# Kernel optimization log

Hardware: AMD Instinct MI355X
Metric: run time of the kernel (lower is better)

## Reference

```python
import jax, jax.numpy as jnp
import numpy as np

N = 50_000        # nodes
E = 1_600_000     # edges (avg degree 32)
H = 64            # hidden_channels
DEPTH = 3         # -> 2*DEPTH mid conv layers


def setup_inputs() -> dict:
    key = jax.random.key(0)
    ks = jax.random.split(key, 8)
    x = jax.random.normal(ks[0], (N, 1), dtype=jnp.float32)
    edge_index = jax.random.randint(ks[1], (2, E), 0, N, dtype=jnp.int32)
    s = 0.1  # small init scale
    W_in = s * jax.random.normal(ks[2], (2 * 1 + 1, H), dtype=jnp.float32)
    b_in = jnp.zeros((H,), jnp.float32)
    W_mid = s * jax.random.normal(ks[3], (2 * DEPTH, 2 * H + 1, H), dtype=jnp.float32)
    b_mid = jnp.zeros((2 * DEPTH, H), jnp.float32)
    W_out = s * jax.random.normal(ks[4], (2 * H + 1, 1), dtype=jnp.float32)
    b_out = jnp.zeros((1,), jnp.float32)
    return {"x": x, "edge_index": edge_index, "W_in": W_in, "b_in": b_in,
            "W_mid": W_mid, "b_mid": b_mid, "W_out": W_out, "b_out": b_out}


def _conv(x, src, dst, sign, inv_deg, W, b):
    """Directional_EdgeConv: mean_{j->i} Linear([x_i, x_j - x_i, sign(j-i)])."""
    x_i = x[dst]                                   # [E, F] target feats
    x_j = x[src]                                   # [E, F] source feats
    feat = jnp.concatenate([x_i, x_j - x_i, sign], axis=-1)  # [E, 2F+1]
    msg = feat @ W + b                             # [E, out]
    agg = jax.ops.segment_sum(msg, dst, num_segments=x.shape[0])  # [N, out]
    return agg * inv_deg                           # mean aggregation


def reference(x, edge_index, W_in, b_in, W_mid, b_mid, W_out, b_out):
    src = edge_index[0]
    dst = edge_index[1]
    # vectorized replacement of the per-edge Python sign loop
    sign = jnp.sign((src - dst).astype(x.dtype))[:, None]        # [E, 1]
    deg = jax.ops.segment_sum(jnp.ones((src.shape[0],), x.dtype), dst,
                              num_segments=x.shape[0])
    inv_deg = (1.0 / jnp.maximum(deg, 1.0))[:, None]             # [N, 1]

    x2 = _conv(x, src, dst, sign, inv_deg, W_in, b_in)
    for l in range(DEPTH):
        x1 = jax.nn.leaky_relu(
            _conv(x2, src, dst, sign, inv_deg, W_mid[2 * l], b_mid[2 * l]))
        x2 = jax.nn.leaky_relu(
            _conv(x1, src, dst, sign, inv_deg, W_mid[2 * l + 1], b_mid[2 * l + 1]) + x2)
    return _conv(x2, src, dst, sign, inv_deg, W_out, b_out) + x
```

## Files before the change

### kernel.cpp

```cpp
#include <hip/hip_runtime.h>
#include <hip/hip_fp16.h>

#define HDIM 64
#define NEG_SLOPE 0.01f
#define CAPB 8192
#define BCAP 6144
#define EPB  4096

typedef _Float16 half8 __attribute__((ext_vector_type(8)));
typedef float f32x4 __attribute__((ext_vector_type(4)));

static __device__ __forceinline__ float h_lo(unsigned d) {
    return __half2float(__ushort_as_half((unsigned short)(d & 0xffffu)));
}
static __device__ __forceinline__ float h_hi(unsigned d) {
    return __half2float(__ushort_as_half((unsigned short)(d >> 16)));
}
static __device__ __forceinline__ unsigned packh(float a, float b) {
    unsigned short ra = __half_as_ushort(__float2half(a));
    unsigned short rb = __half_as_ushort(__float2half(b));
    return ((unsigned)rb << 16) | (unsigned)ra;
}
static __device__ __forceinline__ half8 u4h(uint4 v) {
    union { uint4 u; half8 h; } x; x.u = v; return x.h;
}
static __device__ __forceinline__ __half2 uh2(unsigned u) {
    union { unsigned u; __half2 h; } x; x.u = u; return x.h;
}

__global__ void k_setup(int ptotal, const float* __restrict__ W_mid,
                        unsigned short* __restrict__ WTh,
                        int NB, int* gcur, int N, unsigned* xAP, unsigned* xBP,
                        float* tvec) {
    int i = blockIdx.x * blockDim.x + threadIdx.x;
    if (i < ptotal) {
        int l = i >> 13;
        int rem = i & 8191;
        int h = rem >> 7;
        int k = rem & 127;
        const float* W = W_mid + (size_t)l * 129 * 64;
        float v = W[k * 64 + h] - ((k < 64) ? W[(64 + k) * 64 + h] : 0.f);
        WTh[i] = __half_as_ushort(__float2half(v));
    }
    if (i < NB) gcur[i] = i * CAPB;
    if (i < 32) xAP[(size_t)N * 32 + i] = 0u;
    else if (i < 64) xBP[(size_t)N * 32 + (i - 32)] = 0u;
    else if (i == 64) tvec[N] = 0.f;
}

__global__ __launch_bounds__(1024) void k_bucket(
        int E, const int* __restrict__ src, const int* __restrict__ dst,
        int* gcur, unsigned* __restrict__ bucketed, int NB) {
    __shared__ int lh[512];
    __shared__ int sd[512];
    __shared__ int lbase[512];
    __shared__ unsigned sorted[EPB];
    int t = threadIdx.x;
    int e0 = blockIdx.x * EPB;
    if (t < 512) lh[t] = 0;
    __syncthreads();
    int dv[4], sv[4], rv[4];
#pragma unroll
    for (int k = 0; k < 4; ++k) {
        int e = e0 + k * 1024 + t;
        dv[k] = (e < E) ? dst[e] : -1;
        sv[k] = (e < E) ? src[e] : 0;
    }
#pragma unroll
    for (int k = 0; k < 4; ++k)
        rv[k] = (dv[k] >= 0) ? atomicAdd(&lh[((unsigned)dv[k]) >> 7], 1) : 0;
    __syncthreads();
    int c = (t < 512) ? lh[t] : 0;
    if (t < 512) {
        lbase[t] = (c > 0) ? atomicAdd(&gcur[t], c) : 0;
        sd[t] = c;
    }
    __syncthreads();
    int x = c;
    for (int s = 1; s < 512; s <<= 1) {
        int p = (t < 512 && t >= s) ? sd[t - s] : 0;
        __syncthreads();
        if (t < 512) { x += p; sd[t] = x; }
        __syncthreads();
    }
#pragma unroll
    for (int k = 0; k < 4; ++k) {
        if (dv[k] >= 0) {
            int b = ((unsigned)dv[k]) >> 7;
            sorted[sd[b] - lh[b] + rv[k]] = ((unsigned)dv[k] << 16) | (unsigned)sv[k];
        }
    }
    __syncthreads();
    int ntot = sd[511];
    for (int i = t; i < ntot; i += 1024) {
        unsigned w = sorted[i];
        int b = (int)(w >> 23);
        int pos = lbase[b] + (i - (sd[b] - lh[b]));
        if (pos < (b + 1) * CAPB) bucketed[pos] = w;
    }
}

__global__ __launch_bounds__(512) void k_csr(
        int N, int NB, const unsigned* __restrict__ bucketed, const int* __restrict__ gcur,
        unsigned short* __restrict__ csr, unsigned short* __restrict__ pcsr,
        int* __restrict__ rowptr, float* __restrict__ ssinv) {
    __shared__ unsigned st[BCAP];
    __shared__ int hist[128], cur[128], excl[128], sgp[128];
    __shared__ int gsd[512];
    int b = blockIdx.x, t = threadIdx.x;
    int n0 = b << 7;
    int nn = min(128, N - n0);
    int cc = (t < NB) ? min(gcur[t] - t * CAPB, CAPB) : 0;
    gsd[t] = cc;
    __syncthreads();
    int xs = cc;
    for (int s = 1; s < 512; s <<= 1) {
        int p = (t >= s) ? gsd[t - s] : 0;
        __syncthreads();
        xs += p;
        gsd[t] = xs;
        __syncthreads();
    }
    int cnt = min(gcur[b] - b * CAPB, CAPB);
    int base = gsd[b] - cnt;
    if (b == NB - 1 && t == 0) rowptr[N] = gsd[NB - 1];
    if (t < 128) { hist[t] = 0; sgp[t] = 0; }
    unsigned sent = ((unsigned)N << 16) | (unsigned)N;
    unsigned* pb32 = (unsigned*)(pcsr + ((size_t)b << 13));
    for (int i = t; i < 4096; i += 512) pb32[i] = sent;
    __syncthreads();
    bool single = (cnt <= BCAP);
    for (int off = 0; off < cnt; off += BCAP) {
        int bs = min(BCAP, cnt - off);
        for (int i = t; i < bs; i += 512) {
            unsigned w = bucketed[b * CAPB + off + i];
            if (single) st[i] = w;
            int d = (int)(w >> 16);
            int s = (int)(w & 0xffffu);
            int dl = d - n0;
            atomicAdd(&hist[dl], 1);
            atomicAdd(&sgp[dl], ((s < d) ? 1024 : 0) + ((s == d) ? 1 : 0));
        }
    }
    __syncthreads();
    int deg_t = (t < 128) ? hist[t] : 0;
    int x = deg_t;
    for (int s = 1; s < 128; s <<= 1) {
        int p = (t < 128 && t >= s) ? hist[t - s] : 0;
        __syncthreads();
        if (t < 128) { x += p; hist[t] = x; }
        __syncthreads();
    }
    if (t < 128) {
        int ex = hist[t] - deg_t;
        excl[t] = ex;
        cur[t] = ex;
        if (t < nn) {
            rowptr[n0 + t] = base + ex;
            int sg = sgp[t];
            int lt = sg >> 10, eq = sg & 1023;
            float ss = (float)(deg_t - eq - 2 * lt);
            ssinv[n0 + t] = (deg_t > 0) ? ss / (float)deg_t : 0.f;
        }
    }
    __syncthreads();
    for (int off = 0; off < cnt; off += BCAP) {
        int bs = min(BCAP, cnt - off);
        if (!single) {
            for (int i = t; i < bs; i += 512) st[i] = bucketed[b * CAPB + off + i];
            __syncthreads();
        }
        for (int i = t; i < bs; i += 512) {
            unsigned w = st[i];
            int dl = (int)(w >> 16) - n0;
            unsigned short sval = (unsigned short)(w & 0xffffu);
            int p = atomicAdd(&cur[dl], 1);
            csr[base + p] = sval;
            int r = p - excl[dl];
            if (r < 64) pcsr[((size_t)(n0 + dl) << 6) + r] = sval;
        }
        if (!single) __syncthreads();
    }
}

__global__ void k_in(int N, const float* __restrict__ x0,
                     const int* __restrict__ rowptr, const unsigned short* __restrict__ csr,
                     const float* __restrict__ ssinv,
                     const float* __restrict__ W_in, const float* __restrict__ b_in,
                     unsigned* __restrict__ xoutP) {
    int wid = blockIdx.x * (blockDim.x >> 6) + (threadIdx.x >> 6);
    int lane = threadIdx.x & 63;
    if (wid >= N) return;
    int beg = rowptr[wid], end = rowptr[wid + 1];
    int deg = end - beg;
    float s = 0.f;
    for (int e = beg + lane; e < end; e += 64) s += x0[csr[e]];
    for (int m = 32; m >= 1; m >>= 1) s += __shfl_xor(s, m, 64);
    float invd = 1.f / (float)max(deg, 1);
    float mean = s * invd;
    float xi = x0[wid];
    float w1 = W_in[lane], w2 = W_in[64 + lane], w3 = W_in[128 + lane];
    float y = xi * (w1 - w2) + mean * w2 + ssinv[wid] * w3 + b_in[lane];
    if (deg == 0) y = 0.f;
    float ylo = __shfl(y, (2 * lane) & 63, 64);
    float yhi = __shfl(y, (2 * lane + 1) & 63, 64);
    unsigned pkd = packh(ylo, yhi);
    if (lane < 32) xoutP[(size_t)wid * 32 + lane] = pkd;
}

static __device__ __forceinline__ void chunk_acc(
        const uint4* __restrict__ xin16, int sv, int base, int sub, int lq,
        __half2& c0, __half2& c1, __half2& c2, __half2& c3) {
    int s0 = __shfl(sv, base + sub, 64);
    int s1 = __shfl(sv, base + 8 + sub, 64);
    int s2 = __shfl(sv, base + 16 + sub, 64);
    int s3 = __shfl(sv, base + 24 + sub, 64);
    uint4 d0 = xin16[(size_t)s0 * 8 + lq];
    uint4 d1 = xin16[(size_t)s1 * 8 + lq];
    uint4 d2 = xin16[(size_t)s2 * 8 + lq];
    uint4 d3 = xin16[(size_t)s3 * 8 + lq];
    c0 = __hadd2(c0, __hadd2(__hadd2(uh2(d0.x), uh2(d1.x)), __hadd2(uh2(d2.x), uh2(d3.x))));
    c1 = __hadd2(c1, __hadd2(__hadd2(uh2(d0.y), uh2(d1.y)), __hadd2(uh2(d2.y), uh2(d3.y))));
    c2 = __hadd2(c2, __hadd2(__hadd2(uh2(d0.z), uh2(d1.z)), __hadd2(uh2(d2.z), uh2(d3.z))));
    c3 = __hadd2(c3, __hadd2(__hadd2(uh2(d0.w), uh2(d1.w)), __hadd2(uh2(d2.w), uh2(d3.w))));
}

static __device__ __forceinline__ void slow_gather(
        const uint4* __restrict__ xin16, const unsigned short* __restrict__ csr,
        int beg, int end, int N, int lane, int sub, int lq, float* a) {
#pragma unroll
    for (int j = 0; j < 8; ++j) a[j] = 0.f;
    for (int tb = beg; tb < end; tb += 64) {
        int cnt = min(64, end - tb);
        int sv = (lane < cnt) ? (int)csr[tb + lane] : N;
        int ng = (cnt + 7) >> 3;
        for (int g = 0; g < ng; ++g) {
            int si = __shfl(sv, (g << 3) + sub, 64);
            uint4 d = xin16[(size_t)si * 8 + lq];
            a[0] += h_lo(d.x); a[1] += h_hi(d.x);
            a[2] += h_lo(d.y); a[3] += h_hi(d.y);
            a[4] += h_lo(d.z); a[5] += h_hi(d.z);
            a[6] += h_lo(d.w); a[7] += h_hi(d.w);
        }
    }
#pragma unroll
    for (int m = 8; m <= 32; m <<= 1) {
#pragma unroll
        for (int j = 0; j < 8; ++j) a[j] += __shfl_xor(a[j], m, 64);
    }
}

template <bool RES, bool TOUT>
__global__ __launch_bounds__(256) void k_layer(
        int N, const unsigned* __restrict__ xinP,
        const unsigned* __restrict__ xresP, unsigned* __restrict__ xoutP,
        const int* __restrict__ rowptr, const unsigned short* __restrict__ csr,
        const unsigned short* __restrict__ pcsr,
        const float* __restrict__ ssinv,
        const unsigned short* __restrict__ WThl,
        const float* __restrict__ W3, const float* __restrict__ bias,
        const float* __restrict__ Wt, float* __restrict__ tvec) {
    __shared__ unsigned Ald[16 * 64];
    __shared__ float Cld[16 * 64];
    __shared__ int sdeg[16];
    __shared__ float sss[16];

    int t = threadIdx.x;
    int lane = t & 63;
    int wv = t >> 6;
    int n0 = blockIdx.x << 4;
    int kg = lane >> 4;

    int cb = (wv << 4) + (lane & 15);
    const uint4* wp = (const uint4*)WThl;
    uint4 b0 = wp[cb * 16 + kg + 0];
    uint4 b1 = wp[cb * 16 + kg + 4];
    uint4 b2 = wp[cb * 16 + kg + 8];
    uint4 b3 = wp[cb * 16 + kg + 12];

    const uint4* xin16 = (const uint4*)xinP;
    int sub = lane >> 3;
    int lq = lane & 7;
    int ndb = wv << 2;

    int svp[4];
#pragma unroll
    for (int q = 0; q < 4; ++q)
        svp[q] = (int)pcsr[((size_t)(n0 + ndb + q) << 6) + lane];

#pragma unroll
    for (int qp = 0; qp < 2; ++qp) {
        int ndA = ndb + (qp << 1);
        int ndB = ndA + 1;
        int nodeA = n0 + ndA, nodeB = n0 + ndB;
        int ncA = min(nodeA, N - 1), ncB = min(nodeB, N - 1);
        int begA = __builtin_amdgcn_readfirstlane(rowptr[ncA]);
        int endA = __builtin_amdgcn_readfirstlane(rowptr[ncA + 1]);
        int begB = __builtin_amdgcn_readfirstlane(rowptr[ncB]);
        int endB = __builtin_amdgcn_readfirstlane(rowptr[ncB + 1]);
        int degA = (nodeA < N) ? (endA - begA) : 0;
        int degB = (nodeB < N) ? (endB - begB) : 0;
        float ssvA = ssinv[ncA];
        float ssvB = ssinv[ncB];
        uint4 xiA = make_uint4(0u, 0u, 0u, 0u), xiB = make_uint4(0u, 0u, 0u, 0u);
        if (lane < 8) {
            if (nodeA < N) xiA = xin16[(size_t)ncA * 8 + lane];
            if (nodeB < N) xiB = xin16[(size_t)ncB * 8 + lane];
        }
        uint4 mvA, mvB;
        if (max(degA, degB) <= 64) {
            __half2 z = uh2(0u);
            __half2 cA0 = z, cA1 = z, cA2 = z, cA3 = z;
            __half2 cB0 = z, cB1 = z, cB2 = z, cB3 = z;
            int svA = svp[qp << 1], svB = svp[(qp << 1) + 1];
            chunk_acc(xin16, svA, 0, sub, lq, cA0, cA1, cA2, cA3);
            chunk_acc(xin16, svB, 0, sub, lq, cB0, cB1, cB2, cB3);
            if (degA > 32) chunk_acc(xin16, svA, 32, sub, lq, cA0, cA1, cA2, cA3);
            if (degB > 32) chunk_acc(xin16, svB, 32, sub, lq, cB0, cB1, cB2, cB3);
#pragma unroll
            for (int m = 8; m <= 32; m <<= 1) {
                cA0 = __hadd2(cA0, uh2((unsigned)__shfl_xor((int)*(unsigned*)&cA0, m, 64)));
                cA1 = __hadd2(cA1, uh2((unsigned)__shfl_xor((int)*(unsigned*)&cA1, m, 64)));
                cA2 = __hadd2(cA2, uh2((unsigned)__shfl_xor((int)*(unsigned*)&cA2, m, 64)));
                cA3 = __hadd2(cA3, uh2((unsigned)__shfl_xor((int)*(unsigned*)&cA3, m, 64)));
                cB0 = __hadd2(cB0, uh2((unsigned)__shfl_xor((int)*(unsigned*)&cB0, m, 64)));
                cB1 = __hadd2(cB1, uh2((unsigned)__shfl_xor((int)*(unsigned*)&cB1, m, 64)));
                cB2 = __hadd2(cB2, uh2((unsigned)__shfl_xor((int)*(unsigned*)&cB2, m, 64)));
                cB3 = __hadd2(cB3, uh2((unsigned)__shfl_xor((int)*(unsigned*)&cB3, m, 64)));
            }
            float idA = 1.f / (float)max(degA, 1);
            float idB = 1.f / (float)max(degB, 1);
            mvA.x = packh(__half2float(__low2half(cA0)) * idA, __half2float(__high2half(cA0)) * idA);
            mvA.y = packh(__half2float(__low2half(cA1)) * idA, __half2float(__high2half(cA1)) * idA);
            mvA.z = packh(__half2float(__low2half(cA2)) * idA, __half2float(__high2half(cA2)) * idA);
            mvA.w = packh(__half2float(__low2half(cA3)) * idA, __half2float(__high2half(cA3)) * idA);
            mvB.x = packh(__half2float(__low2half(cB0)) * idB, __half2float(__high2half(cB0)) * idB);
            mvB.y = packh(__half2float(__low2half(cB1)) * idB, __half2float(__high2half(cB1)) * idB);
            mvB.z = packh(__half2float(__low2half(cB2)) * idB, __half2float(__high2half(cB2)) * idB);
            mvB.w = packh(__half2float(__low2half(cB3)) * idB, __half2float(__high2half(cB3)) * idB);
        } else {
            float aA[8], aB[8];
            slow_gather(xin16, csr, begA, endA, N, lane, sub, lq, aA);
            slow_gather(xin16, csr, begB, endB, N, lane, sub, lq, aB);
            float idA = 1.f / (float)max(degA, 1);
            float idB = 1.f / (float)max(degB, 1);
            mvA.x = packh(aA[0] * idA, aA[1] * idA);
            mvA.y = packh(aA[2] * idA, aA[3] * idA);
            mvA.z = packh(aA[4] * idA, aA[5] * idA);
            mvA.w = packh(aA[6] * idA, aA[7] * idA);
            mvB.x = packh(aB[0] * idB, aB[1] * idB);
            mvB.y = packh(aB[2] * idB, aB[3] * idB);
            mvB.z = packh(aB[4] * idB, aB[5] * idB);
            mvB.w = packh(aB[6] * idB, aB[7] * idB);
        }
        if (lane < 8) {
            int gxA = lane ^ (ndA & 7), gmA = (8 + lane) ^ (ndA & 7);
            int gxB = lane ^ (ndB & 7), gmB = (8 + lane) ^ (ndB & 7);
            ((uint4*)Ald)[ndA * 16 + gxA] = xiA;
            ((uint4*)Ald)[ndA * 16 + gmA] = mvA;
            ((uint4*)Ald)[ndB * 16 + gxB] = xiB;
            ((uint4*)Ald)[ndB * 16 + gmB] = mvB;
        }
        if (lane == 0) {
            sdeg[ndA] = degA; sss[ndA] = ssvA;
            sdeg[ndB] = degB; sss[ndB] = ssvB;
        }
    }
    __syncthreads();

    int r = lane & 15;
    const uint4* ap = (const uint4*)Ald;
    int rx = (r & 7);
    uint4 fa0 = ap[r * 16 + ((0 + kg) ^ rx)];
    uint4 fa1 = ap[r * 16 + ((4 + kg) ^ rx)];
    uint4 fa2 = ap[r * 16 + ((8 + kg) ^ rx)];
    uint4 fa3 = ap[r * 16 + ((12 + kg) ^ rx)];
    f32x4 acc = {0.f, 0.f, 0.f, 0.f};
    acc = __builtin_amdgcn_mfma_f32_16x16x32_f16(u4h(fa0), u4h(b0), acc, 0, 0, 0);
    acc = __builtin_amdgcn_mfma_f32_16x16x32_f16(u4h(fa1), u4h(b1), acc, 0, 0, 0);
    acc = __builtin_amdgcn_mfma_f32_16x16x32_f16(u4h(fa2), u4h(b2), acc, 0, 0, 0);
    acc = __builtin_amdgcn_mfma_f32_16x16x32_f16(u4h(fa3), u4h(b3), acc, 0, 0, 0);
#pragma unroll
    for (int reg = 0; reg < 4; ++reg)
        Cld[(kg * 4 + reg) * 64 + (wv << 4) + r] = acc[reg];
    __syncthreads();

    int nd = t >> 4;
    int node = n0 + nd;
    if (node < N) {
        int dg = sdeg[nd];
        float ss = sss[nd];
        float tp = 0.f;
#pragma unroll
        for (int jj = 0; jj < 2; ++jj) {
            int j = (t & 15) + jj * 16;
            float y0 = Cld[nd * 64 + 2 * j];
            float y1 = Cld[nd * 64 + 2 * j + 1];
            float2 w3 = ((const float2*)W3)[j];
            float2 bb = ((const float2*)bias)[j];
            y0 += ss * w3.x + bb.x;
            y1 += ss * w3.y + bb.y;
            if (dg == 0) { y0 = 0.f; y1 = 0.f; }
            if (RES) {
                unsigned rw = xresP[(size_t)node * 32 + j];
                y0 += h_lo(rw);
                y1 += h_hi(rw);
            }
            y0 = (y0 > 0.f) ? y0 : NEG_SLOPE * y0;
            y1 = (y1 > 0.f) ? y1 : NEG_SLOPE * y1;
            if (TOUT) {
                float2 wt = ((const float2*)Wt)[j];
                tp += y0 * wt.x + y1 * wt.y;
            }
            xoutP[(size_t)node * 32 + j] = packh(y0, y1);
        }
        if (TOUT) {
            tp += __shfl_xor(tp, 1, 64);
            tp += __shfl_xor(tp, 2, 64);
            tp += __shfl_xor(tp, 4, 64);
            tp += __shfl_xor(tp, 8, 64);
            if ((t & 15) == 0) tvec[node] = tp;
        }
    }
}

__global__ void k_out(int N, const unsigned* __restrict__ xAP, const float* __restrict__ x0,
                      const int* __restrict__ rowptr, const unsigned short* __restrict__ csr,
                      const unsigned short* __restrict__ pcsr,
                      const float* __restrict__ ssinv, const float* __restrict__ t,
                      const float* __restrict__ W_out, const float* __restrict__ b_out,
                      float* __restrict__ out) {
    int wid = blockIdx.x * (blockDim.x >> 6) + (threadIdx.x >> 6);
    int lane = threadIdx.x & 63;
    if (wid >= N) return;
    int beg = rowptr[wid], end = rowptr[wid + 1];
    int deg = end - beg;
    float s;
    if (deg <= 64) {
        int sl = (int)pcsr[((size_t)wid << 6) + lane];
        s = t[sl];
    } else {
        s = 0.f;
        for (int e = beg + lane; e < end; e += 64) s += t[csr[e]];
    }
    unsigned xw = xAP[(size_t)wid * 32 + (lane >> 1)];
    float xf = (lane & 1) ? h_hi(xw) : h_lo(xw);
    float p = xf * (W_out[lane] - W_out[64 + lane]);
    for (int m = 32; m >= 1; m >>= 1) {
        s += __shfl_xor(s, m, 64);
        p += __shfl_xor(p, m, 64);
    }
    float invd = 1.f / (float)max(deg, 1);
    float y = p + s * invd + ssinv[wid] * W_out[128] + b_out[0];
    if (deg == 0) y = 0.f;
    if (lane == 0) out[wid] = y + x0[wid];
}

static inline size_t align16(size_t x) { return (x + 15) & ~(size_t)15; }

extern "C" void kernel_launch(void* const* d_in, const int* in_sizes, int n_in,
                              void* d_out, int out_size, void* d_ws, size_t ws_size,
                              hipStream_t stream) {
    const float* x0    = (const float*)d_in[0];
    const int*   ei    = (const int*)d_in[1];
    const float* W_in  = (const float*)d_in[2];
    const float* b_in  = (const float*)d_in[3];
    const float* W_mid = (const float*)d_in[4];
    const float* b_mid = (const float*)d_in[5];
    const float* W_out = (const float*)d_in[6];
    const float* b_out = (const float*)d_in[7];
    float* out = (float*)d_out;

    const int N = in_sizes[0];
    const int E = in_sizes[1] / 2;
    const int L = in_sizes[4] / (129 * 64);
    const int NB = (N + 127) >> 7;
    const int* src = ei;
    const int* dst = ei + E;

    char* p = (char*)d_ws;
    unsigned short* WTh = (unsigned short*)p; p += align16((size_t)L * 64 * 128 * 2);
    unsigned* xAP = (unsigned*)p; p += align16((size_t)(N + 1) * 32 * 4);
    unsigned* xBP = (unsigned*)p; p += align16((size_t)(N + 1) * 32 * 4);
    unsigned* bucketed = (unsigned*)p; p += align16((size_t)NB * CAPB * 4);
    unsigned short* csr = (unsigned short*)p; p += align16((size_t)E * 2);
    unsigned short* pcsr = (unsigned short*)p; p += align16((size_t)NB * 8192 * 2);
    int* gcur          = (int*)p; p += align16((size_t)(NB + 1) * 4);
    int* rowptr        = (int*)p; p += align16((size_t)(N + 1) * 4);
    float* ssinv       = (float*)p; p += align16((size_t)N * 4);
    float* t           = (float*)p; p += align16((size_t)(N + 1) * 4);

    const int nb_w4 = (N + 3) / 4;
    const int nb_bkt = (E + EPB - 1) / EPB;
    const int ptotal = L * 64 * 128;
    const int nb_lay = (N + 15) / 16;

    k_setup<<<(ptotal + 255) / 256, 256, 0, stream>>>(ptotal, W_mid, WTh, NB, gcur, N, xAP, xBP, t);
    k_bucket<<<nb_bkt, 1024, 0, stream>>>(E, src, dst, gcur, bucketed, NB);
    k_csr<<<NB, 512, 0, stream>>>(N, NB, bucketed, gcur, csr, pcsr, rowptr, ssinv);

    k_in<<<nb_w4, 256, 0, stream>>>(N, x0, rowptr, csr, ssinv, W_in, b_in, xAP);

    for (int l = 0; l < L / 2; ++l) {
        bool last = (l == L / 2 - 1);
        const unsigned short* Wa = WTh + (size_t)(2 * l) * 64 * 128;
        const unsigned short* Wb = WTh + (size_t)(2 * l + 1) * 64 * 128;
        const float* W3a = W_mid + (size_t)(2 * l) * 129 * 64 + 128 * 64;
        const float* W3b = W_mid + (size_t)(2 * l + 1) * 129 * 64 + 128 * 64;

        k_layer<false, false><<<nb_lay, 256, 0, stream>>>(
            N, xAP, nullptr, xBP, rowptr, csr, pcsr, ssinv,
            Wa, W3a, b_mid + (size_t)(2 * l) * HDIM, nullptr, nullptr);
        if (!last) {
            k_layer<true, false><<<nb_lay, 256, 0, stream>>>(
                N, xBP, xAP, xAP, rowptr, csr, pcsr, ssinv,
                Wb, W3b, b_mid + (size_t)(2 * l + 1) * HDIM, nullptr, nullptr);
        } else {
            k_layer<true, true><<<nb_lay, 256, 0, stream>>>(
                N, xBP, xAP, xAP, rowptr, csr, pcsr, ssinv,
                Wb, W3b, b_mid + (size_t)(2 * l + 1) * HDIM, W_out + 64, t);
        }
    }

    k_out<<<nb_w4, 256, 0, stream>>>(N, xAP, x0, rowptr, csr, pcsr, ssinv, t,
                                     W_out, b_out, out);
}
```

Measured before the change: 242.5 us.

## Fuse input conv layer into CSR build kernel using shared-memory padded CSR

Merges the k_in kernel into k_csr. The padded 64-slot neighbor list is built in LDS and copied to global with vector stores instead of scattered 2-byte writes. Each block then computes the input-layer conv for its 128 nodes from the LDS copy, which removes one launch and the reread of rowptr, csr and ssinv. It adds 16KB of LDS per block and serializes 16 nodes per wave, which may lower occupancy in k_csr.

```diff
diff --git a/kernel.cpp b/kernel.cpp
--- a/kernel.cpp
+++ b/kernel.cpp
@@ -103,9 +103,13 @@
 __global__ __launch_bounds__(512) void k_csr(
         int N, int NB, const unsigned* __restrict__ bucketed, const int* __restrict__ gcur,
         unsigned short* __restrict__ csr, unsigned short* __restrict__ pcsr,
-        int* __restrict__ rowptr, float* __restrict__ ssinv) {
+        int* __restrict__ rowptr, float* __restrict__ ssinv,
+        const float* __restrict__ x0, const float* __restrict__ W_in,
+        const float* __restrict__ b_in, unsigned* __restrict__ xAP) {
     __shared__ unsigned st[BCAP];
-    __shared__ int hist[128], cur[128], excl[128], sgp[128];
+    __shared__ unsigned short lpcsr[128 * 64];
+    __shared__ int hist[128], cur[128], excl[128], sgp[128], sdegl[128];
+    __shared__ float sssl[128];
     __shared__ int gsd[512];
     int b = blockIdx.x, t = threadIdx.x;
     int n0 = b << 7;
@@ -126,8 +130,7 @@
     if (b == NB - 1 && t == 0) rowptr[N] = gsd[NB - 1];
     if (t < 128) { hist[t] = 0; sgp[t] = 0; }
     unsigned sent = ((unsigned)N << 16) | (unsigned)N;
-    unsigned* pb32 = (unsigned*)(pcsr + ((size_t)b << 13));
-    for (int i = t; i < 4096; i += 512) pb32[i] = sent;
+    for (int i = t; i < 4096; i += 512) ((unsigned*)lpcsr)[i] = sent;
     __syncthreads();
     bool single = (cnt <= BCAP);
     for (int off = 0; off < cnt; off += BCAP) {
@@ -155,13 +158,17 @@
         int ex = hist[t] - deg_t;
         excl[t] = ex;
         cur[t] = ex;
+        sdegl[t] = deg_t;
+        float ssv = 0.f;
         if (t < nn) {
             rowptr[n0 + t] = base + ex;
             int sg = sgp[t];
             int lt = sg >> 10, eq = sg & 1023;
             float ss = (float)(deg_t - eq - 2 * lt);
-            ssinv[n0 + t] = (deg_t > 0) ? ss / (float)deg_t : 0.f;
-        }
+            ssv = (deg_t > 0) ? ss / (float)deg_t : 0.f;
+            ssinv[n0 + t] = ssv;
+        }
+        sssl[t] = ssv;
     }
     __syncthreads();
     for (int off = 0; off < cnt; off += BCAP) {
@@ -177,35 +184,44 @@
             int p = atomicAdd(&cur[dl], 1);
             csr[base + p] = sval;
             int r = p - excl[dl];
-            if (r < 64) pcsr[((size_t)(n0 + dl) << 6) + r] = sval;
+            if (r < 64) lpcsr[(dl << 6) + r] = sval;
         }
         if (!single) __syncthreads();
     }
-}
-
-__global__ void k_in(int N, const float* __restrict__ x0,
-                     const int* __restrict__ rowptr, const unsigned short* __restrict__ csr,
-                     const float* __restrict__ ssinv,
-                     const float* __restrict__ W_in, const float* __restrict__ b_in,
-                     unsigned* __restrict__ xoutP) {
-    int wid = blockIdx.x * (blockDim.x >> 6) + (threadIdx.x >> 6);
-    int lane = threadIdx.x & 63;
-    if (wid >= N) return;
-    int beg = rowptr[wid], end = rowptr[wid + 1];
-    int deg = end - beg;
-    float s = 0.f;
-    for (int e = beg + lane; e < end; e += 64) s += x0[csr[e]];
-    for (int m = 32; m >= 1; m >>= 1) s += __shfl_xor(s, m, 64);
-    float invd = 1.f / (float)max(deg, 1);
-    float mean = s * invd;
-    float xi = x0[wid];
+    __syncthreads();
+    {
+        uint4* gp = (uint4*)(pcsr + ((size_t)b << 13));
+        const uint4* lp = (const uint4*)lpcsr;
+        for (int i = t; i < 1024; i += 512) gp[i] = lp[i];
+    }
+    int lane = t & 63;
+    int wvq = t >> 6;
     float w1 = W_in[lane], w2 = W_in[64 + lane], w3 = W_in[128 + lane];
-    float y = xi * (w1 - w2) + mean * w2 + ssinv[wid] * w3 + b_in[lane];
-    if (deg == 0) y = 0.f;
-    float ylo = __shfl(y, (2 * lane) & 63, 64);
-    float yhi = __shfl(y, (2 * lane + 1) & 63, 64);
-    unsigned pkd = packh(ylo, yhi);
-    if (lane < 32) xoutP[(size_t)wid * 32 + lane] = pkd;
+    float bi = b_in[lane];
+    for (int i = 0; i < 16; ++i) {
+        int nd = (wvq << 4) + i;
+        int node = n0 + nd;
+        if (node >= N) break;
+        int deg = sdegl[nd];
+        float s;
+        if (deg <= 64) {
+            int sl = (int)lpcsr[(nd << 6) + lane];
+            s = (sl < N) ? x0[sl] : 0.f;
+        } else {
+            s = 0.f;
+            int bg = base + excl[nd], en = bg + deg;
+            for (int e = bg + lane; e < en; e += 64) s += x0[csr[e]];
+        }
+        for (int m = 32; m >= 1; m >>= 1) s += __shfl_xor(s, m, 64);
+        float invd = 1.f / (float)max(deg, 1);
+        float mean = s * invd;
+        float xi = x0[node];
+        float y = xi * (w1 - w2) + mean * w2 + sssl[nd] * w3 + bi;
+        if (deg == 0) y = 0.f;
+        float ylo = __shfl(y, (2 * lane) & 63, 64);
+        float yhi = __shfl(y, (2 * lane + 1) & 63, 64);
+        if (lane < 32) xAP[(size_t)node * 32 + lane] = packh(ylo, yhi);
+    }
 }
 
 static __device__ __forceinline__ void chunk_acc(
@@ -497,9 +513,8 @@
 
     k_setup<<<(ptotal + 255) / 256, 256, 0, stream>>>(ptotal, W_mid, WTh, NB, gcur, N, xAP, xBP, t);
     k_bucket<<<nb_bkt, 1024, 0, stream>>>(E, src, dst, gcur, bucketed, NB);
-    k_csr<<<NB, 512, 0, stream>>>(N, NB, bucketed, gcur, csr, pcsr, rowptr, ssinv);
-
-    k_in<<<nb_w4, 256, 0, stream>>>(N, x0, rowptr, csr, ssinv, W_in, b_in, xAP);
+    k_csr<<<NB, 512, 0, stream>>>(N, NB, bucketed, gcur, csr, pcsr, rowptr, ssinv,
+                                  x0, W_in, b_in, xAP);
 
     for (int l = 0; l < L / 2; ++l) {
         bool last = (l == L / 2 - 1);
```

Result: faster. 234.5 us (median of 2 runs) (-3.3%).
